# Optimization experiments

Hardware: AMD Instinct MI355X
Metric: run time of the kernel (lower is better)

The kernel has to match this reference:

```python
import jax, jax.numpy as jnp
import numpy as np


def setup_inputs() -> dict:
    key = jax.random.key(0)
    B, C, T = 64, 256, 2048
    X = jax.random.normal(key, (B, C, T), dtype=jnp.float32)
    return {"X": X}


def reference(X) -> jnp.ndarray:
    # torch.cov(correction=0) per sample: rows = variables, cols = observations
    T = X.shape[-1]
    Xc = X - jnp.mean(X, axis=-1, keepdims=True)      # [B, C, T]
    cov = jnp.einsum('bct,bdt->bcd', Xc, Xc) / T       # [B, C, C]
    return cov
```

## Files before the change

### kernel.cpp

```cpp
#include <hip/hip_runtime.h>


#define NB 64
#define NC 256
#define NT 2048
#define BK 64
#define NITER 16

typedef __bf16 bf16x8 __attribute__((ext_vector_type(8)));
typedef float  f32x8  __attribute__((ext_vector_type(8)));
typedef float  f32x4  __attribute__((ext_vector_type(4)));

__global__ __launch_bounds__(512, 2) void cov_kernel(const float* __restrict__ X,
                                                     float* __restrict__ out) {
    __shared__ __align__(16) unsigned char smem[131072];
    char*  sbase = (char*)smem;
    float* redF  = (float*)smem;

    const int bid  = blockIdx.x;
    const int xcd  = bid & 7;
    const int g    = bid >> 3;
    const int b    = xcd + 8 * (g >> 2);
    const int q    = g & 3;
    const int row0 = (q >> 1) * 128, col0 = (q & 1) * 128;

    const float* __restrict__ Xb = X + (size_t)b * (NC * NT);

    const int t    = threadIdx.x;
    const int lane = t & 63;
    const int wave = t >> 6;
    const int h    = wave >> 2;
    const int wq   = wave & 3;
    const int wm   = wq >> 1, wn = wq & 1;
    const int quad = lane >> 4;
    const int l16  = lane & 15;

    const int u   = t & 255;
    const int sr  = u >> 1;
    const int scf = (u & 1) * 32;
    const float* gA = Xb + (size_t)(row0 + sr) * NT + h * (NT / 2) + scf;
    const float* gB = Xb + (size_t)(col0 + sr) * NT + h * (NT / 2) + scf;

    char* pa[2] = { sbase +         (0 * 2 + h) * 16384,
                    sbase +         (1 * 2 + h) * 16384 };
    char* pb[2] = { sbase + 65536 + (0 * 2 + h) * 16384,
                    sbase + 65536 + (1 * 2 + h) * 16384 };

    int wOff[4];
#pragma unroll
    for (int j = 0; j < 4; ++j)
        wOff[j] = (sr * 128 + scf * 2 + j * 16) ^ ((sr & 7) << 4);

    const int aB0 = ((wm * 64 + l16) * 128 + quad * 16) ^ ((l16 & 7) << 4);
    const int bB0 = ((wn * 64 + l16) * 128 + quad * 16) ^ ((l16 & 7) << 4);

    f32x4 acc[4][4], accRS[4], accCS[4];
#pragma unroll
    for (int i = 0; i < 4; ++i) {
        accRS[i] = (f32x4){0.f, 0.f, 0.f, 0.f};
        accCS[i] = (f32x4){0.f, 0.f, 0.f, 0.f};
#pragma unroll
        for (int j = 0; j < 4; ++j) acc[i][j] = (f32x4){0.f, 0.f, 0.f, 0.f};
    }
    const bf16x8 ones = {(__bf16)1.0f, (__bf16)1.0f, (__bf16)1.0f, (__bf16)1.0f,
                         (__bf16)1.0f, (__bf16)1.0f, (__bf16)1.0f, (__bf16)1.0f};

    f32x8 pA[4], pB[4];
#pragma unroll
    for (int j = 0; j < 4; ++j) {
        pA[j] = *(const f32x8*)(gA + j * 8);
        pB[j] = *(const f32x8*)(gB + j * 8);
    }
#pragma unroll
    for (int j = 0; j < 4; ++j) {
        *(bf16x8*)(pa[0] + wOff[j]) = __builtin_convertvector(pA[j], bf16x8);
        *(bf16x8*)(pb[0] + wOff[j]) = __builtin_convertvector(pB[j], bf16x8);
    }
#pragma unroll
    for (int j = 0; j < 4; ++j) {
        pA[j] = *(const f32x8*)(gA + BK + j * 8);
        pB[j] = *(const f32x8*)(gB + BK + j * 8);
    }
    __syncthreads();

#pragma unroll 2
    for (int k = 0; k < NITER; ++k) {
        const int cur = k & 1, nxt = cur ^ 1;

        if (k + 1 < NITER) {
#pragma unroll
            for (int j = 0; j < 4; ++j) {
                *(bf16x8*)(pa[nxt] + wOff[j]) = __builtin_convertvector(pA[j], bf16x8);
                *(bf16x8*)(pb[nxt] + wOff[j]) = __builtin_convertvector(pB[j], bf16x8);
            }
        }
        if (k + 2 < NITER) {
#pragma unroll
            for (int j = 0; j < 4; ++j) {
                pA[j] = *(const f32x8*)(gA + (k + 2) * BK + j * 8);
                pB[j] = *(const f32x8*)(gB + (k + 2) * BK + j * 8);
            }
        }

#pragma unroll
        for (int ksub = 0; ksub < 2; ++ksub) {
            bf16x8 aF[4], bF[4];
#pragma unroll
            for (int mt = 0; mt < 4; ++mt)
                aF[mt] = *(const bf16x8*)(pa[cur] + ((aB0 + mt * 2048) ^ (ksub << 6)));
#pragma unroll
            for (int nt = 0; nt < 4; ++nt)
                bF[nt] = *(const bf16x8*)(pb[cur] + ((bB0 + nt * 2048) ^ (ksub << 6)));

#pragma unroll
            for (int mt = 0; mt < 4; ++mt) {
                accRS[mt] = __builtin_amdgcn_mfma_f32_16x16x32_bf16(aF[mt], ones, accRS[mt], 0, 0, 0);
#pragma unroll
                for (int nt = 0; nt < 4; ++nt)
                    acc[mt][nt] = __builtin_amdgcn_mfma_f32_16x16x32_bf16(aF[mt], bF[nt], acc[mt][nt], 0, 0, 0);
            }
#pragma unroll
            for (int nt = 0; nt < 4; ++nt)
                accCS[nt] = __builtin_amdgcn_mfma_f32_16x16x32_bf16(ones, bF[nt], accCS[nt], 0, 0, 0);
        }

        __syncthreads();
    }

    float* red = redF + wq * (64 * 65);
    float* rs  = redF + 4 * (64 * 65);
    float* cs  = rs + 256;

    if (h == 1) {
#pragma unroll
        for (int mt = 0; mt < 4; ++mt)
#pragma unroll
            for (int nt = 0; nt < 4; ++nt)
#pragma unroll
                for (int r = 0; r < 4; ++r)
                    red[(mt * 16 + quad * 4 + r) * 65 + nt * 16 + l16] = acc[mt][nt][r];
        if (l16 == 0) {
#pragma unroll
            for (int mt = 0; mt < 4; ++mt)
#pragma unroll
                for (int r = 0; r < 4; ++r)
                    rs[wq * 64 + mt * 16 + quad * 4 + r] = accRS[mt][r];
        }
        if (quad == 0) {
#pragma unroll
            for (int nt = 0; nt < 4; ++nt)
                cs[wq * 64 + nt * 16 + l16] = accCS[nt][0];
        }
    }
    __syncthreads();

    if (h == 0) {
        const float invT = 1.0f / NT;
        float* __restrict__ outB = out + (size_t)b * (NC * NC);
#pragma unroll
        for (int mt = 0; mt < 4; ++mt) {
#pragma unroll
            for (int nt = 0; nt < 4; ++nt) {
#pragma unroll
                for (int r = 0; r < 4; ++r) {
                    const int R = mt * 16 + quad * 4 + r;
                    const int C = nt * 16 + l16;
                    const float tot = red[R * 65 + C] + acc[mt][nt][r];
                    const float Sx  = rs[wq * 64 + R] + accRS[mt][r];
                    const float Sy  = cs[wq * 64 + C] + accCS[nt][0];
                    outB[(size_t)(row0 + wm * 64 + R) * NC + (col0 + wn * 64 + C)] =
                        (tot - Sx * Sy * invT) * invT;
                }
            }
        }
    }
}

extern "C" void kernel_launch(void* const* d_in, const int* in_sizes, int n_in,
                              void* d_out, int out_size, void* d_ws, size_t ws_size,
                              hipStream_t stream) {
    const float* X = (const float*)d_in[0];
    float* out = (float*)d_out;
    (void)in_sizes; (void)n_in; (void)out_size; (void)d_ws; (void)ws_size;
    cov_kernel<<<256, 512, 0, stream>>>(X, out);
}
```

Measured before the change: 219.3 us.

## Exploit covariance symmetry: split off-diagonal tile over K and mirror in fixup kernel

```diff
diff --git a/kernel.cpp b/kernel.cpp
--- a/kernel.cpp
+++ b/kernel.cpp
@@ -5,14 +5,15 @@
 #define NC 256
 #define NT 2048
 #define BK 64
-#define NITER 16
+#define WSB 33280
 
 typedef __bf16 bf16x8 __attribute__((ext_vector_type(8)));
 typedef float  f32x8  __attribute__((ext_vector_type(8)));
 typedef float  f32x4  __attribute__((ext_vector_type(4)));
 
-__global__ __launch_bounds__(512, 2) void cov_kernel(const float* __restrict__ X,
-                                                     float* __restrict__ out) {
+__global__ __launch_bounds__(512, 2) void cov_gram(const float* __restrict__ X,
+                                                   float* __restrict__ out,
+                                                   float* __restrict__ ws) {
     __shared__ __align__(16) unsigned char smem[131072];
     char*  sbase = (char*)smem;
     float* redF  = (float*)smem;
@@ -21,8 +22,8 @@
     const int xcd  = bid & 7;
     const int g    = bid >> 3;
     const int b    = xcd + 8 * (g >> 2);
-    const int q    = g & 3;
-    const int row0 = (q >> 1) * 128, col0 = (q & 1) * 128;
+    const int role = g & 3;
+    const bool diag = (role < 2);
 
     const float* __restrict__ Xb = X + (size_t)b * (NC * NT);
 
@@ -35,22 +36,28 @@
     const int quad = lane >> 4;
     const int l16  = lane & 15;
 
+    const int niter = diag ? 16 : 8;
+    const int kb    = diag ? h * 1024 : (role & 1) * 1024 + h * 512;
+    const int ar0   = diag ? role * 128 : 0;
+
     const int u   = t & 255;
     const int sr  = u >> 1;
     const int scf = (u & 1) * 32;
-    const float* gA = Xb + (size_t)(row0 + sr) * NT + h * (NT / 2) + scf;
-    const float* gB = Xb + (size_t)(col0 + sr) * NT + h * (NT / 2) + scf;
-
-    char* pa[2] = { sbase +         (0 * 2 + h) * 16384,
-                    sbase +         (1 * 2 + h) * 16384 };
-    char* pb[2] = { sbase + 65536 + (0 * 2 + h) * 16384,
-                    sbase + 65536 + (1 * 2 + h) * 16384 };
+    const float* gA = Xb + (size_t)(ar0 + sr) * NT + kb + scf;
+    const float* gB = Xb + (size_t)(128 + sr) * NT + kb + scf;
+
+    char* pa[2] = { sbase + (0 * 2 + h) * 16384, sbase + (1 * 2 + h) * 16384 };
+    char* pb[2];
+    if (diag) { pb[0] = pa[0]; pb[1] = pa[1]; }
+    else {
+        pb[0] = sbase + 65536 + (0 * 2 + h) * 16384;
+        pb[1] = sbase + 65536 + (1 * 2 + h) * 16384;
+    }
 
     int wOff[4];
 #pragma unroll
     for (int j = 0; j < 4; ++j)
         wOff[j] = (sr * 128 + scf * 2 + j * 16) ^ ((sr & 7) << 4);
-
     const int aB0 = ((wm * 64 + l16) * 128 + quad * 16) ^ ((l16 & 7) << 4);
     const int bB0 = ((wn * 64 + l16) * 128 + quad * 16) ^ ((l16 & 7) << 4);
 
@@ -67,38 +74,49 @@
 
     f32x8 pA[4], pB[4];
 #pragma unroll
-    for (int j = 0; j < 4; ++j) {
-        pA[j] = *(const f32x8*)(gA + j * 8);
-        pB[j] = *(const f32x8*)(gB + j * 8);
-    }
-#pragma unroll
-    for (int j = 0; j < 4; ++j) {
+    for (int j = 0; j < 4; ++j) pA[j] = *(const f32x8*)(gA + j * 8);
+    if (!diag) {
+#pragma unroll
+        for (int j = 0; j < 4; ++j) pB[j] = *(const f32x8*)(gB + j * 8);
+    }
+#pragma unroll
+    for (int j = 0; j < 4; ++j)
         *(bf16x8*)(pa[0] + wOff[j]) = __builtin_convertvector(pA[j], bf16x8);
-        *(bf16x8*)(pb[0] + wOff[j]) = __builtin_convertvector(pB[j], bf16x8);
-    }
-#pragma unroll
-    for (int j = 0; j < 4; ++j) {
-        pA[j] = *(const f32x8*)(gA + BK + j * 8);
-        pB[j] = *(const f32x8*)(gB + BK + j * 8);
+    if (!diag) {
+#pragma unroll
+        for (int j = 0; j < 4; ++j)
+            *(bf16x8*)(pb[0] + wOff[j]) = __builtin_convertvector(pB[j], bf16x8);
+    }
+#pragma unroll
+    for (int j = 0; j < 4; ++j) pA[j] = *(const f32x8*)(gA + BK + j * 8);
+    if (!diag) {
+#pragma unroll
+        for (int j = 0; j < 4; ++j) pB[j] = *(const f32x8*)(gB + BK + j * 8);
     }
     __syncthreads();
 
 #pragma unroll 2
-    for (int k = 0; k < NITER; ++k) {
+    for (int k = 0; k < niter; ++k) {
         const int cur = k & 1, nxt = cur ^ 1;
 
-        if (k + 1 < NITER) {
-#pragma unroll
-            for (int j = 0; j < 4; ++j) {
+        if (k + 1 < niter) {
+#pragma unroll
+            for (int j = 0; j < 4; ++j)
                 *(bf16x8*)(pa[nxt] + wOff[j]) = __builtin_convertvector(pA[j], bf16x8);
-                *(bf16x8*)(pb[nxt] + wOff[j]) = __builtin_convertvector(pB[j], bf16x8);
-            }
-        }
-        if (k + 2 < NITER) {
-#pragma unroll
-            for (int j = 0; j < 4; ++j) {
+            if (!diag) {
+#pragma unroll
+                for (int j = 0; j < 4; ++j)
+                    *(bf16x8*)(pb[nxt] + wOff[j]) = __builtin_convertvector(pB[j], bf16x8);
+            }
+        }
+        if (k + 2 < niter) {
+#pragma unroll
+            for (int j = 0; j < 4; ++j)
                 pA[j] = *(const f32x8*)(gA + (k + 2) * BK + j * 8);
-                pB[j] = *(const f32x8*)(gB + (k + 2) * BK + j * 8);
+            if (!diag) {
+#pragma unroll
+                for (int j = 0; j < 4; ++j)
+                    pB[j] = *(const f32x8*)(gB + (k + 2) * BK + j * 8);
             }
         }
 
@@ -155,24 +173,104 @@
     __syncthreads();
 
     if (h == 0) {
-        const float invT = 1.0f / NT;
-        float* __restrict__ outB = out + (size_t)b * (NC * NC);
-#pragma unroll
-        for (int mt = 0; mt < 4; ++mt) {
-#pragma unroll
-            for (int nt = 0; nt < 4; ++nt) {
-#pragma unroll
-                for (int r = 0; r < 4; ++r) {
-                    const int R = mt * 16 + quad * 4 + r;
+        if (diag) {
+            const float invT = 1.0f / NT;
+            const int row0 = role * 128, col0 = role * 128;
+            float* __restrict__ outB = out + (size_t)b * (NC * NC);
+#pragma unroll
+            for (int mt = 0; mt < 4; ++mt) {
+#pragma unroll
+                for (int nt = 0; nt < 4; ++nt) {
+#pragma unroll
+                    for (int r = 0; r < 4; ++r) {
+                        const int R = mt * 16 + quad * 4 + r;
+                        const int C = nt * 16 + l16;
+                        const float tot = red[R * 65 + C] + acc[mt][nt][r];
+                        const float Sx  = rs[wq * 64 + R] + accRS[mt][r];
+                        const float Sy  = cs[wq * 64 + C] + accCS[nt][0];
+                        outB[(size_t)(row0 + wm * 64 + R) * NC + (col0 + wn * 64 + C)] =
+                            (tot - Sx * Sy * invT) * invT;
+                    }
+                }
+            }
+        } else {
+            const int half = role & 1;
+            float* __restrict__ wsP = ws + (size_t)b * WSB + (size_t)half * 16384;
+            float* __restrict__ sxW = ws + (size_t)b * WSB + 32768 + half * 128;
+            float* __restrict__ syW = ws + (size_t)b * WSB + 33024 + half * 128;
+#pragma unroll
+            for (int mt = 0; mt < 4; ++mt) {
+#pragma unroll
+                for (int nt = 0; nt < 4; ++nt) {
+#pragma unroll
+                    for (int r = 0; r < 4; ++r) {
+                        const int R = mt * 16 + quad * 4 + r;
+                        const int C = nt * 16 + l16;
+                        wsP[(size_t)(wm * 64 + R) * 128 + wn * 64 + C] =
+                            red[R * 65 + C] + acc[mt][nt][r];
+                    }
+                }
+            }
+            if (l16 == 0 && wn == 0) {
+#pragma unroll
+                for (int mt = 0; mt < 4; ++mt)
+#pragma unroll
+                    for (int r = 0; r < 4; ++r) {
+                        const int R = mt * 16 + quad * 4 + r;
+                        sxW[wm * 64 + R] = rs[wq * 64 + R] + accRS[mt][r];
+                    }
+            }
+            if (quad == 0 && wm == 0) {
+#pragma unroll
+                for (int nt = 0; nt < 4; ++nt) {
                     const int C = nt * 16 + l16;
-                    const float tot = red[R * 65 + C] + acc[mt][nt][r];
-                    const float Sx  = rs[wq * 64 + R] + accRS[mt][r];
-                    const float Sy  = cs[wq * 64 + C] + accCS[nt][0];
-                    outB[(size_t)(row0 + wm * 64 + R) * NC + (col0 + wn * 64 + C)] =
-                        (tot - Sx * Sy * invT) * invT;
+                    syW[wn * 64 + C] = cs[wq * 64 + C] + accCS[nt][0];
                 }
             }
         }
+    }
+}
+
+__global__ __launch_bounds__(256) void cov_fix(const float* __restrict__ ws,
+                                               float* __restrict__ out) {
+    __shared__ float tile[32][133];
+    const int bid = blockIdx.x;
+    const int b   = bid >> 2;
+    const int c0  = (bid & 3) * 32;
+    const float* __restrict__ wsB = ws + (size_t)b * WSB;
+    const float* __restrict__ P0  = wsB;
+    const float* __restrict__ P1  = wsB + 16384;
+    const float* sx0 = wsB + 32768; const float* sx1 = sx0 + 128;
+    const float* sy0 = wsB + 33024; const float* sy1 = sy0 + 128;
+    float* __restrict__ outB = out + (size_t)b * (NC * NC);
+    const float invT = 1.0f / NT;
+    const int tid = threadIdx.x;
+
+#pragma unroll
+    for (int j = 0; j < 4; ++j) {
+        const int idx = tid + j * 256;
+        const int ri  = idx >> 5;
+        const int c4  = (idx & 31) * 4;
+        const int R   = c0 + ri;
+        f32x4 s = *(const f32x4*)&P0[(size_t)R * 128 + c4];
+        s += *(const f32x4*)&P1[(size_t)R * 128 + c4];
+        const float Sx = sx0[R] + sx1[R];
+        f32x4 Sy = *(const f32x4*)&sy0[c4];
+        Sy += *(const f32x4*)&sy1[c4];
+        const f32x4 v = (s - Sy * (Sx * invT)) * invT;
+        *(f32x4*)&outB[(size_t)R * NC + 128 + c4] = v;
+        tile[ri][c4 + 0] = v[0]; tile[ri][c4 + 1] = v[1];
+        tile[ri][c4 + 2] = v[2]; tile[ri][c4 + 3] = v[3];
+    }
+    __syncthreads();
+#pragma unroll
+    for (int j = 0; j < 4; ++j) {
+        const int idx = tid + j * 256;
+        const int mr  = idx >> 3;
+        const int mc  = (idx & 7) * 4;
+        const f32x4 v = { tile[mc + 0][mr], tile[mc + 1][mr],
+                          tile[mc + 2][mr], tile[mc + 3][mr] };
+        *(f32x4*)&outB[(size_t)(128 + mr) * NC + c0 + mc] = v;
     }
 }
 
@@ -181,6 +279,8 @@
                               hipStream_t stream) {
     const float* X = (const float*)d_in[0];
     float* out = (float*)d_out;
-    (void)in_sizes; (void)n_in; (void)out_size; (void)d_ws; (void)ws_size;
-    cov_kernel<<<256, 512, 0, stream>>>(X, out);
+    float* ws = (float*)d_ws;
+    (void)in_sizes; (void)n_in; (void)out_size; (void)ws_size;
+    cov_gram<<<256, 512, 0, stream>>>(X, out, ws);
+    cov_fix<<<256, 256, 0, stream>>>(ws, out);
 }
```

Result: faster. 211.1 us (-3.7%).
